# Kernel optimization log

Measured on AMD Instinct MI355X. Metric: run time of the kernel, lower is better.

## Reference

```python
import jax, jax.numpy as jnp
import numpy as np

NQ = 12          # num_qubits
NL = 5           # num_layers
NA = 4           # num_actions
DIM = 2 ** NQ    # state-vector dimension

# PennyLane convention: wire 0 is the most-significant bit of the state index.
_idx = np.arange(DIM)
_bits = (_idx[:, None] >> (NQ - 1 - np.arange(NQ))) & 1           # [DIM, NQ]
_cz = np.ones(DIM)
for _i in range(NQ):                                              # ring of CZs (all diagonal -> fuse)
    _cz *= np.where((_bits[:, _i] & _bits[:, (_i + 1) % NQ]) == 1, -1.0, 1.0)
CZ_RING = jnp.asarray(_cz, dtype=jnp.complex64)                   # [DIM]
ZTAB = jnp.asarray(1 - 2 * _bits[:, :NA], dtype=jnp.float32)      # [DIM, NA] PauliZ eigenvalues


def _bc(v):
    # broadcast an angle-derived scalar or [B] vector against [B, lead, trail]
    v = jnp.asarray(v)
    return v.reshape(v.shape + (1, 1))


def _apply_1q(state, wire, m00, m01, m10, m11):
    b = state.shape[0]
    lead, trail = 2 ** wire, 2 ** (NQ - 1 - wire)
    s = state.reshape(b, lead, 2, trail)
    s0, s1 = s[:, :, 0, :], s[:, :, 1, :]
    return jnp.stack([m00 * s0 + m01 * s1, m10 * s0 + m11 * s1], axis=2).reshape(b, DIM)


def _rx(state, wire, theta):
    c = _bc(jnp.cos(0.5 * theta)).astype(jnp.complex64)
    s = _bc(jnp.sin(0.5 * theta)).astype(jnp.complex64)
    return _apply_1q(state, wire, c, -1j * s, -1j * s, c)


def _ry(state, wire, theta):
    c = _bc(jnp.cos(0.5 * theta)).astype(jnp.complex64)
    s = _bc(jnp.sin(0.5 * theta)).astype(jnp.complex64)
    return _apply_1q(state, wire, c, -s, s, c)


def _rz(state, wire, theta):
    # diagonal gate: no mixing across the wire axis
    b = state.shape[0]
    lead, trail = 2 ** wire, 2 ** (NQ - 1 - wire)
    e = _bc(jnp.exp(-0.5j * theta))  # e^{-i t/2}; conj(e) = e^{+i t/2} for real t
    s = state.reshape(b, lead, 2, trail)
    return jnp.stack([e * s[:, :, 0, :], jnp.conj(e) * s[:, :, 1, :]], axis=2).reshape(b, DIM)


def setup_inputs() -> dict:
    key = jax.random.key(0)
    k1, k2 = jax.random.split(key)
    x = jax.random.normal(k1, (4096, 4 * NQ), dtype=jnp.float32)
    input_scaling = jnp.ones((NL, 3, NQ), dtype=jnp.float32)
    weights = jax.random.uniform(k2, (NL, 3, 2 * NQ), dtype=jnp.float32,
                                 minval=-np.pi, maxval=np.pi)
    output_scaling = jnp.ones((NA,), dtype=jnp.float32)
    return {"x": x, "input_scaling": input_scaling, "weights": weights,
            "output_scaling": output_scaling}


def reference(x, input_scaling, weights, output_scaling):
    b = x.shape[0]
    feats = (x[:, NQ:2 * NQ], x[:, 2 * NQ:3 * NQ], x[:, 3 * NQ:4 * NQ])
    state = jnp.zeros((b, DIM), dtype=jnp.complex64).at[:, 0].set(1.0)
    for layer in range(NL):
        for blk in range(3):
            f = feats[blk]
            for i in range(NQ):
                state = _rx(state, i, input_scaling[layer, blk, i] * f[:, i])
            for i in range(NQ):
                state = _ry(state, i, weights[layer, blk, i])
            for i in range(NQ):
                state = _rz(state, i, weights[layer, blk, i + NQ])
            state = state * CZ_RING[None, :]
    probs = state.real ** 2 + state.imag ** 2          # [B, DIM]
    expvals = probs @ ZTAB                             # [B, NA] <Z_i>
    return expvals * output_scaling                    # logits
```

## Files before the change

### kernel.cpp

```cpp
#include <hip/hip_runtime.h>
#include <stdint.h>

#define NQ 12
#define NL 5
#define NIT 15
#define AMPS 16
#define CPB (NIT * NQ)


typedef float f2 __attribute__((ext_vector_type(2)));

static __device__ __forceinline__ float f_u(unsigned u) { return __uint_as_float(u); }
static __device__ __forceinline__ unsigned u_f(float f) { return __float_as_uint(f); }

#define PK_MUL_RR(acc, C, S) \
    asm("v_pk_mul_f32 %0, %1, %2 op_sel_hi:[0,1]" : "=v"(acc) : "v"(C), "v"(S))
#define PK_FMA_I(acc, C, S) \
    asm("v_pk_fma_f32 %0, %1, %2, %0 op_sel:[1,1,0] op_sel_hi:[1,0,1] neg_lo:[1,0,0]" \
        : "+v"(acc) : "v"(C), "v"(S))
#define PK_FMA_R(acc, C, S) \
    asm("v_pk_fma_f32 %0, %1, %2, %0 op_sel_hi:[0,1,1]" : "+v"(acc) : "v"(C), "v"(S))
#define PK_FMA_IC(acc, C, S) \
    asm("v_pk_fma_f32 %0, %1, %2, %0 op_sel:[1,1,0] op_sel_hi:[1,0,1] neg_hi:[1,0,0]" \
        : "+v"(acc) : "v"(C), "v"(S))
#define PK_FMA_RN(acc, C, S) \
    asm("v_pk_fma_f32 %0, %1, %2, %0 op_sel_hi:[0,1,1] neg_lo:[1,0,0] neg_hi:[1,0,0]" \
        : "+v"(acc) : "v"(C), "v"(S))

#define CPLX_AB(DST, CA, S, CB, O)                                    \
    { f2 t_;                                                          \
      PK_MUL_RR(t_, CA, S); PK_FMA_I(t_, CA, S);                      \
      PK_FMA_R (t_, CB, O); PK_FMA_I(t_, CB, O);                      \
      DST = t_; }

template <int CTRL>
static __device__ __forceinline__ float dpp_xor(float v) {
    int u = (int)__float_as_uint(v);
    return __uint_as_float((unsigned)__builtin_amdgcn_update_dpp(u, u, CTRL, 0xF, 0xF, false));
}
static __device__ __forceinline__ float swz_xor4(float v) {
    return f_u((unsigned)__builtin_amdgcn_ds_swizzle((int)u_f(v), 0x101F));
}

#define AB_GATE_PK(OPX)                                                 \
    _Pragma("unroll")                                                   \
    for (int r = 0; r < AMPS; ++r) {                                    \
        f2 o; o.x = OPX(s[r].x); o.y = OPX(s[r].y);                     \
        CPLX_AB(s[r], CA, s[r], CB, o)                                  \
    }

template <int ST>
static __device__ __forceinline__ void reg_gate_pk(f2 (&s)[AMPS], f2 CAg, f2 CBg) {
#pragma unroll
    for (int r0 = 0; r0 < AMPS; ++r0) {
        if (r0 & ST) continue;
        const int r1 = r0 | ST;
        const f2 s0 = s[r0], s1 = s[r1];
        f2 t0, t1;
        PK_MUL_RR(t0, CAg, s0); PK_FMA_I (t0, CAg, s0);
        PK_FMA_R (t0, CBg, s1); PK_FMA_I (t0, CBg, s1);
        PK_MUL_RR(t1, CAg, s1); PK_FMA_IC(t1, CAg, s1);
        PK_FMA_RN(t1, CBg, s0); PK_FMA_I (t1, CBg, s0);
        s[r0] = t0; s[r1] = t1;
    }
}

static __device__ __forceinline__ float4 build_coef(float alpha, float beta, float gamma) {
    float sa, ca, sb, cb, sg, cg;
    sincosf(0.5f * alpha, &sa, &ca);
    sincosf(0.5f * beta,  &sb, &cb);
    sincosf(0.5f * gamma, &sg, &cg);
    float cbca = cb * ca, sbsa = sb * sa, sbca = sb * ca, cbsa = cb * sa;
    float ar =  cg * cbca + sg * sbsa;
    float ai =  cg * sbsa - sg * cbca;
    float br = -(cg * sbca + sg * cbsa);
    float bi =  sg * sbca - cg * cbsa;
    return make_float4(ar, ai, br, bi);
}

__global__ __launch_bounds__(256) void coef_kernel(
    const float* __restrict__ x, const float* __restrict__ iscale,
    const float* __restrict__ w, float4* __restrict__ ctab, int total)
{
    int gid = blockIdx.x * 256 + threadIdx.x;
    if (gid >= total) return;
    int b  = gid / CPB;
    int t  = gid - b * CPB;
    int it = t / NQ;
    int q  = t - it * NQ;
    int blk = it - 3 * (it / 3);
    float f     = x[(size_t)b * (4 * NQ) + NQ + blk * NQ + q];
    float alpha = iscale[it * NQ + q] * f;
    ctab[gid] = build_coef(alpha, w[it * 2 * NQ + q], w[it * 2 * NQ + NQ + q]);
}

template <bool TAB>
__global__ __launch_bounds__(256) void qsim_kernel(
    const float* __restrict__ x,
    const float* __restrict__ iscale,
    const float* __restrict__ w,
    const float* __restrict__ oscale,
    const float4* __restrict__ ctab,
    float* __restrict__ out)
{
    const int tid  = threadIdx.x;
    const int lane = tid & 63;
    const int wv   = tid >> 6;
    const int b    = blockIdx.x;

    extern __shared__ float4 smem[];
    float4* buf  = smem;
    float4* clds = smem + 1536;

#define TBUF(SLOT, Q) buf[((((SLOT) << 1) | (Q)) << 6) | lane]

    if constexpr (!TAB) {
        if (tid < CPB) {
            const int it  = tid / NQ;
            const int q   = tid - it * NQ;
            const int blk = it - 3 * (it / 3);
            float f     = x[(size_t)b * (4 * NQ) + NQ + blk * NQ + q];
            float alpha = iscale[it * NQ + q] * f;
            clds[tid] = build_coef(alpha, w[it * 2 * NQ + q], w[it * 2 * NQ + NQ + q]);
        }
        __syncthreads();
    }

    f2 s[AMPS];
#pragma unroll
    for (int r = 0; r < AMPS; ++r) { s[r].x = 0.f; s[r].y = 0.f; }
    if (tid == 0) s[0].x = 1.f;

    unsigned czmA = 0, czmB = 0;
#pragma unroll
    for (int r = 0; r < AMPS; ++r) {
        unsigned ia = ((unsigned)wv << 10) | ((unsigned)lane << 4) | (unsigned)r;
        unsigned ib = (((unsigned)(r >> 3) & 1u) << 11) | (((unsigned)(r >> 2) & 1u) << 10)
                    | ((unsigned)lane << 4)
                    | (((unsigned)(wv >> 1) & 1u) << 3) | (((unsigned)wv & 1u) << 2)
                    | ((unsigned)r & 3u);
        unsigned pa = ((unsigned)__popc((ia & (ia >> 1)) & 0x7FFu) + ((ia & (ia >> 11)) & 1u)) & 1u;
        unsigned pb = ((unsigned)__popc((ib & (ib >> 1)) & 0x7FFu) + ((ib & (ib >> 11)) & 1u)) & 1u;
        czmA |= pa << r;
        czmB |= pb << r;
    }

    const bool hb2 = (lane >> 5) & 1;
    const bool hb3 = (lane >> 4) & 1;
    const unsigned sb4 = (unsigned)((lane >> 3) & 1) << 31;
    const unsigned sb5 = (unsigned)((lane >> 2) & 1) << 31;
    const unsigned sb6 = (unsigned)((lane >> 1) & 1) << 31;
    const unsigned sb7 = (unsigned)(lane & 1) << 31;

    const float4* gtab = TAB ? (ctab + (size_t)b * CPB) : nullptr;

#pragma unroll 1
    for (int it = 0; it < NIT; ++it) {
        float4 c[NQ];
        if constexpr (TAB) {
#pragma unroll
            for (int q = 0; q < NQ; ++q) c[q] = gtab[it * NQ + q];
        } else {
#pragma unroll
            for (int q = 0; q < NQ; ++q) c[q] = clds[it * NQ + q];
        }
        const bool ev = (it & 1) == 0;

        {
            const float4 c0 = ev ? c[8] : c[0];
            const float4 c1 = ev ? c[9] : c[1];
            { const f2 CA = { c0.x, c0.y }, CB = { c0.z, c0.w }; reg_gate_pk<8>(s, CA, CB); }
            { const f2 CA = { c1.x, c1.y }, CB = { c1.z, c1.w }; reg_gate_pk<4>(s, CA, CB); }
            { const f2 CA = { c[10].x, c[10].y }, CB = { c[10].z, c[10].w }; reg_gate_pk<2>(s, CA, CB); }
            { const f2 CA = { c[11].x, c[11].y }, CB = { c[11].z, c[11].w }; reg_gate_pk<1>(s, CA, CB); }
        }

        {
            const f2 CP = { hb2 ? -c[2].z : c[2].x, hb2 ?  c[2].w : c[2].y };
            const f2 CQ = { hb2 ?  c[2].x : c[2].z, hb2 ? -c[2].y : c[2].w };
#pragma unroll
            for (int r = 0; r < AMPS; ++r) {
                auto dx = __builtin_amdgcn_permlane32_swap(u_f(s[r].x), u_f(s[r].x), false, false);
                auto dy = __builtin_amdgcn_permlane32_swap(u_f(s[r].y), u_f(s[r].y), false, false);
                f2 na = { f_u(dx[0]), f_u(dy[0]) };
                f2 nb = { f_u(dx[1]), f_u(dy[1]) };
                CPLX_AB(s[r], CP, na, CQ, nb)
            }
        }
        {
            const f2 CP = { hb3 ? -c[3].z : c[3].x, hb3 ?  c[3].w : c[3].y };
            const f2 CQ = { hb3 ?  c[3].x : c[3].z, hb3 ? -c[3].y : c[3].w };
#pragma unroll
            for (int r = 0; r < AMPS; ++r) {
                auto dx = __builtin_amdgcn_permlane16_swap(u_f(s[r].x), u_f(s[r].x), false, false);
                auto dy = __builtin_amdgcn_permlane16_swap(u_f(s[r].y), u_f(s[r].y), false, false);
                f2 na = { f_u(dx[0]), f_u(dy[0]) };
                f2 nb = { f_u(dx[1]), f_u(dy[1]) };
                CPLX_AB(s[r], CP, na, CQ, nb)
            }
        }
        {
            const f2 CA = { c[4].x, f_u(u_f(c[4].y) ^ sb4) };
            const f2 CB = { f_u(u_f(c[4].z) ^ sb4), c[4].w };
            AB_GATE_PK(dpp_xor<0x128>)
        }
        {
            const f2 CA = { c[5].x, f_u(u_f(c[5].y) ^ sb5) };
            const f2 CB = { f_u(u_f(c[5].z) ^ sb5), c[5].w };
#pragma unroll
            for (int h = 0; h < 2; ++h) {
                float ox[8], oy[8];
#pragma unroll
                for (int r = 0; r < 8; ++r) {
                    ox[r] = swz_xor4(s[h*8 + r].x);
                    oy[r] = swz_xor4(s[h*8 + r].y);
                }
#pragma unroll
                for (int r = 0; r < 8; ++r) {
                    f2 o = { ox[r], oy[r] };
                    CPLX_AB(s[h*8 + r], CA, s[h*8 + r], CB, o)
                }
            }
        }
        {
            const f2 CA = { c[6].x, f_u(u_f(c[6].y) ^ sb6) };
            const f2 CB = { f_u(u_f(c[6].z) ^ sb6), c[6].w };
            AB_GATE_PK(dpp_xor<0x4E>)
        }
        {
            const f2 CA = { c[7].x, f_u(u_f(c[7].y) ^ sb7) };
            const f2 CB = { f_u(u_f(c[7].z) ^ sb7), c[7].w };
            AB_GATE_PK(dpp_xor<0xB1>)
        }

        __syncthreads();
#pragma unroll
        for (int g = 0; g < 4; ++g) {
            if (g == wv) continue;
            const int slot = g * 3 + (wv < g ? wv : wv - 1);
            TBUF(slot, 0) = make_float4(s[4*g+0].x, s[4*g+0].y, s[4*g+1].x, s[4*g+1].y);
            TBUF(slot, 1) = make_float4(s[4*g+2].x, s[4*g+2].y, s[4*g+3].x, s[4*g+3].y);
        }
        __syncthreads();
#pragma unroll
        for (int h = 0; h < 4; ++h) {
            if (h == wv) continue;
            const int slot = wv * 3 + (h < wv ? h : h - 1);
            const float4 pa = TBUF(slot, 0);
            const float4 pb = TBUF(slot, 1);
            s[4*h+0] = f2{ pa.x, pa.y }; s[4*h+1] = f2{ pa.z, pa.w };
            s[4*h+2] = f2{ pb.x, pb.y }; s[4*h+3] = f2{ pb.z, pb.w };
        }

        {
            const float4 c0 = ev ? c[0] : c[8];
            const float4 c1 = ev ? c[1] : c[9];
            { const f2 CA = { c0.x, c0.y }, CB = { c0.z, c0.w }; reg_gate_pk<8>(s, CA, CB); }
            { const f2 CA = { c1.x, c1.y }, CB = { c1.z, c1.w }; reg_gate_pk<4>(s, CA, CB); }
        }

        const unsigned mcz = ev ? czmB : czmA;
#pragma unroll
        for (int r = 0; r < AMPS; ++r) {
            const unsigned sgn = ((mcz >> r) & 1u) << 31;
            s[r].x = f_u(u_f(s[r].x) ^ sgn);
            s[r].y = f_u(u_f(s[r].y) ^ sgn);
        }
    }

    float pg[4];
#pragma unroll
    for (int g = 0; g < 4; ++g) {
        float p = 0.f;
#pragma unroll
        for (int j = 0; j < 4; ++j)
            p = fmaf(s[4*g+j].x, s[4*g+j].x, fmaf(s[4*g+j].y, s[4*g+j].y, p));
        pg[g] = p;
    }
    const float ptot = (pg[0] + pg[1]) + (pg[2] + pg[3]);
    float v0 = (pg[0] + pg[1]) - (pg[2] + pg[3]);
    float v1 = (pg[0] + pg[2]) - (pg[1] + pg[3]);
    float v2 = hb2 ? -ptot : ptot;
    float v3 = hb3 ? -ptot : ptot;
#pragma unroll
    for (int m = 1; m <= 32; m <<= 1) {
        v0 += __shfl_xor(v0, m);
        v1 += __shfl_xor(v1, m);
        v2 += __shfl_xor(v2, m);
        v3 += __shfl_xor(v3, m);
    }

    __syncthreads();
    if (lane == 0) buf[wv] = make_float4(v0, v1, v2, v3);
    __syncthreads();
    if (tid == 0) {
        float4 a0 = buf[0], a1 = buf[1], a2 = buf[2], a3 = buf[3];
        float4 o;
        o.x = (a0.x + a1.x + a2.x + a3.x) * oscale[0];
        o.y = (a0.y + a1.y + a2.y + a3.y) * oscale[1];
        o.z = (a0.z + a1.z + a2.z + a3.z) * oscale[2];
        o.w = (a0.w + a1.w + a2.w + a3.w) * oscale[3];
        *reinterpret_cast<float4*>(out + (size_t)b * 4) = o;
    }
#undef TBUF
}

extern "C" void kernel_launch(void* const* d_in, const int* in_sizes, int n_in,
                              void* d_out, int out_size, void* d_ws, size_t ws_size,
                              hipStream_t stream) {
    const float* x      = (const float*)d_in[0];
    const float* iscale = (const float*)d_in[1];
    const float* w      = (const float*)d_in[2];
    const float* oscale = (const float*)d_in[3];
    float* out          = (float*)d_out;

    const int batch = in_sizes[0] / (4 * NQ);
    const size_t need = (size_t)batch * CPB * sizeof(float4);

    if (ws_size >= need) {
        const int total = batch * CPB;
        coef_kernel<<<(total + 255) / 256, 256, 0, stream>>>(x, iscale, w, (float4*)d_ws, total);
        qsim_kernel<true><<<batch, 256, 12 * 2 * 64 * sizeof(float4), stream>>>(
            x, iscale, w, oscale, (const float4*)d_ws, out);
    } else {
        qsim_kernel<false><<<batch, 256, (12 * 2 * 64 + CPB) * sizeof(float4), stream>>>(
            x, iscale, w, oscale, nullptr, out);
    }
}
```

Baseline: 568.8 us.

## Use 128-thread blocks with 32 amplitudes per thread and analytic first layer

Result: faster. 543.8 us (-4.4%).

```diff
diff --git a/kernel.cpp b/kernel.cpp
--- a/kernel.cpp
+++ b/kernel.cpp
@@ -2,9 +2,8 @@
 #include <stdint.h>
 
 #define NQ 12
-#define NL 5
 #define NIT 15
-#define AMPS 16
+#define AMPS 32
 #define CPB (NIT * NQ)
 
 
@@ -27,6 +26,9 @@
     asm("v_pk_fma_f32 %0, %1, %2, %0 op_sel_hi:[0,1,1] neg_lo:[1,0,0] neg_hi:[1,0,0]" \
         : "+v"(acc) : "v"(C), "v"(S))
 
+#define CMUL(DST, CA, CB) \
+    { PK_MUL_RR(DST, CA, CB); PK_FMA_I(DST, CA, CB); }
+
 #define CPLX_AB(DST, CA, S, CB, O)                                    \
     { f2 t_;                                                          \
       PK_MUL_RR(t_, CA, S); PK_FMA_I(t_, CA, S);                      \
@@ -78,29 +80,15 @@
     return make_float4(ar, ai, br, bi);
 }
 
-__global__ __launch_bounds__(256) void coef_kernel(
-    const float* __restrict__ x, const float* __restrict__ iscale,
-    const float* __restrict__ w, float4* __restrict__ ctab, int total)
-{
-    int gid = blockIdx.x * 256 + threadIdx.x;
-    if (gid >= total) return;
-    int b  = gid / CPB;
-    int t  = gid - b * CPB;
-    int it = t / NQ;
-    int q  = t - it * NQ;
-    int blk = it - 3 * (it / 3);
-    float f     = x[(size_t)b * (4 * NQ) + NQ + blk * NQ + q];
-    float alpha = iscale[it * NQ + q] * f;
-    ctab[gid] = build_coef(alpha, w[it * 2 * NQ + q], w[it * 2 * NQ + NQ + q]);
-}
-
-template <bool TAB>
-__global__ __launch_bounds__(256) void qsim_kernel(
+static __device__ __forceinline__ f2 usel(float4 c, int bit) {
+    return bit ? f2{ -c.z, c.w } : f2{ c.x, c.y };
+}
+
+__global__ __launch_bounds__(128) void qsim_kernel(
     const float* __restrict__ x,
     const float* __restrict__ iscale,
     const float* __restrict__ w,
     const float* __restrict__ oscale,
-    const float4* __restrict__ ctab,
     float* __restrict__ out)
 {
     const int tid  = threadIdx.x;
@@ -108,76 +96,98 @@
     const int wv   = tid >> 6;
     const int b    = blockIdx.x;
 
-    extern __shared__ float4 smem[];
-    float4* buf  = smem;
-    float4* clds = smem + 1536;
-
-#define TBUF(SLOT, Q) buf[((((SLOT) << 1) | (Q)) << 6) | lane]
-
-    if constexpr (!TAB) {
-        if (tid < CPB) {
-            const int it  = tid / NQ;
-            const int q   = tid - it * NQ;
-            const int blk = it - 3 * (it / 3);
-            float f     = x[(size_t)b * (4 * NQ) + NQ + blk * NQ + q];
-            float alpha = iscale[it * NQ + q] * f;
-            clds[tid] = build_coef(alpha, w[it * 2 * NQ + q], w[it * 2 * NQ + NQ + q]);
-        }
-        __syncthreads();
-    }
-
-    f2 s[AMPS];
-#pragma unroll
-    for (int r = 0; r < AMPS; ++r) { s[r].x = 0.f; s[r].y = 0.f; }
-    if (tid == 0) s[0].x = 1.f;
+    __shared__ float4 buf[8 * 128];
+    __shared__ float4 clds[CPB];
+
+    for (int t = tid; t < CPB; t += 128) {
+        const int it  = t / NQ;
+        const int q   = t - it * NQ;
+        const int blk = it - 3 * (it / 3);
+        float f     = x[(size_t)b * (4 * NQ) + NQ + blk * NQ + q];
+        float alpha = iscale[it * NQ + q] * f;
+        clds[t] = build_coef(alpha, w[it * 2 * NQ + q], w[it * 2 * NQ + NQ + q]);
+    }
 
     unsigned czmA = 0, czmB = 0;
 #pragma unroll
     for (int r = 0; r < AMPS; ++r) {
-        unsigned ia = ((unsigned)wv << 10) | ((unsigned)lane << 4) | (unsigned)r;
-        unsigned ib = (((unsigned)(r >> 3) & 1u) << 11) | (((unsigned)(r >> 2) & 1u) << 10)
-                    | ((unsigned)lane << 4)
-                    | (((unsigned)(wv >> 1) & 1u) << 3) | (((unsigned)wv & 1u) << 2)
-                    | ((unsigned)r & 3u);
+        unsigned ia = ((unsigned)wv << 11) | ((unsigned)lane << 5) | (unsigned)r;
+        unsigned ib = (((unsigned)r >> 4) << 11) | ((unsigned)lane << 5)
+                    | ((unsigned)wv << 4) | ((unsigned)r & 15u);
         unsigned pa = ((unsigned)__popc((ia & (ia >> 1)) & 0x7FFu) + ((ia & (ia >> 11)) & 1u)) & 1u;
         unsigned pb = ((unsigned)__popc((ib & (ib >> 1)) & 0x7FFu) + ((ib & (ib >> 11)) & 1u)) & 1u;
         czmA |= pa << r;
         czmB |= pb << r;
     }
 
-    const bool hb2 = (lane >> 5) & 1;
-    const bool hb3 = (lane >> 4) & 1;
-    const unsigned sb4 = (unsigned)((lane >> 3) & 1) << 31;
-    const unsigned sb5 = (unsigned)((lane >> 2) & 1) << 31;
-    const unsigned sb6 = (unsigned)((lane >> 1) & 1) << 31;
-    const unsigned sb7 = (unsigned)(lane & 1) << 31;
-
-    const float4* gtab = TAB ? (ctab + (size_t)b * CPB) : nullptr;
+    const bool hbW1 = (lane >> 5) & 1;
+    const bool hbW2 = (lane >> 4) & 1;
+    const unsigned sbW3 = (unsigned)((lane >> 3) & 1) << 31;
+    const unsigned sbW4 = (unsigned)((lane >> 2) & 1) << 31;
+    const unsigned sbW5 = (unsigned)((lane >> 1) & 1) << 31;
+    const unsigned sbW6 = (unsigned)(lane & 1) << 31;
+
+    __syncthreads();
+
+    f2 s[AMPS];
+
+    {
+        float4 c0 = clds[0], c1 = clds[1], c2 = clds[2],  c3 = clds[3];
+        float4 c4 = clds[4], c5 = clds[5], c6 = clds[6],  c7 = clds[7];
+        float4 c8 = clds[8], c9 = clds[9], cA = clds[10], cB = clds[11];
+
+        f2 tc = usel(c1, (lane >> 5) & 1);
+        { f2 u = usel(c2, (lane >> 4) & 1); f2 t; CMUL(t, tc, u) tc = t; }
+        { f2 u = usel(c3, (lane >> 3) & 1); f2 t; CMUL(t, tc, u) tc = t; }
+        { f2 u = usel(c4, (lane >> 2) & 1); f2 t; CMUL(t, tc, u) tc = t; }
+        { f2 u = usel(c5, (lane >> 1) & 1); f2 t; CMUL(t, tc, u) tc = t; }
+        { f2 u = usel(c6, lane & 1);        f2 t; CMUL(t, tc, u) tc = t; }
+        { f2 u = usel(c7, wv);              f2 t; CMUL(t, tc, u) tc = t; }
+        f2 tc0, tc1;
+        { f2 u = usel(c0, 0); CMUL(tc0, tc, u) }
+        { f2 u = usel(c0, 1); CMUL(tc1, tc, u) }
+
+        f2 pA[4], pB[4], plow[16];
+#pragma unroll
+        for (int j = 0; j < 4; ++j) {
+            f2 u8 = usel(c8, j >> 1), u9 = usel(c9, j & 1);
+            CMUL(pA[j], u8, u9)
+            f2 uA = usel(cA, j >> 1), uB = usel(cB, j & 1);
+            CMUL(pB[j], uA, uB)
+        }
+#pragma unroll
+        for (int m = 0; m < 16; ++m) CMUL(plow[m], pA[m >> 2], pB[m & 3])
+#pragma unroll
+        for (int r = 0; r < AMPS; ++r) CMUL(s[r], (r < 16 ? tc0 : tc1), plow[r & 15])
+
+#pragma unroll
+        for (int r = 0; r < AMPS; ++r) {
+            const unsigned sgn = ((czmB >> r) & 1u) << 31;
+            s[r].x = f_u(u_f(s[r].x) ^ sgn);
+            s[r].y = f_u(u_f(s[r].y) ^ sgn);
+        }
+    }
 
 #pragma unroll 1
-    for (int it = 0; it < NIT; ++it) {
-        float4 c[NQ];
-        if constexpr (TAB) {
-#pragma unroll
-            for (int q = 0; q < NQ; ++q) c[q] = gtab[it * NQ + q];
-        } else {
-#pragma unroll
-            for (int q = 0; q < NQ; ++q) c[q] = clds[it * NQ + q];
-        }
+    for (int it = 1; it < NIT; ++it) {
+        const float4* cit = clds + it * NQ;
         const bool ev = (it & 1) == 0;
 
-        {
-            const float4 c0 = ev ? c[8] : c[0];
-            const float4 c1 = ev ? c[9] : c[1];
-            { const f2 CA = { c0.x, c0.y }, CB = { c0.z, c0.w }; reg_gate_pk<8>(s, CA, CB); }
-            { const f2 CA = { c1.x, c1.y }, CB = { c1.z, c1.w }; reg_gate_pk<4>(s, CA, CB); }
-            { const f2 CA = { c[10].x, c[10].y }, CB = { c[10].z, c[10].w }; reg_gate_pk<2>(s, CA, CB); }
-            { const f2 CA = { c[11].x, c[11].y }, CB = { c[11].z, c[11].w }; reg_gate_pk<1>(s, CA, CB); }
-        }
-
-        {
-            const f2 CP = { hb2 ? -c[2].z : c[2].x, hb2 ?  c[2].w : c[2].y };
-            const f2 CQ = { hb2 ?  c[2].x : c[2].z, hb2 ? -c[2].y : c[2].w };
+        { float4 cf = cit[ev ? 7 : 0];
+          const f2 CA = { cf.x, cf.y }, CB = { cf.z, cf.w }; reg_gate_pk<16>(s, CA, CB); }
+        { float4 cc = cit[8];
+          const f2 CA = { cc.x, cc.y }, CB = { cc.z, cc.w }; reg_gate_pk<8>(s, CA, CB); }
+        { float4 cc = cit[9];
+          const f2 CA = { cc.x, cc.y }, CB = { cc.z, cc.w }; reg_gate_pk<4>(s, CA, CB); }
+        { float4 cc = cit[10];
+          const f2 CA = { cc.x, cc.y }, CB = { cc.z, cc.w }; reg_gate_pk<2>(s, CA, CB); }
+        { float4 cc = cit[11];
+          const f2 CA = { cc.x, cc.y }, CB = { cc.z, cc.w }; reg_gate_pk<1>(s, CA, CB); }
+
+        {
+            float4 cc = cit[1];
+            const f2 CP = { hbW1 ? -cc.z : cc.x, hbW1 ?  cc.w : cc.y };
+            const f2 CQ = { hbW1 ?  cc.x : cc.z, hbW1 ? -cc.y : cc.w };
 #pragma unroll
             for (int r = 0; r < AMPS; ++r) {
                 auto dx = __builtin_amdgcn_permlane32_swap(u_f(s[r].x), u_f(s[r].x), false, false);
@@ -188,8 +198,9 @@
             }
         }
         {
-            const f2 CP = { hb3 ? -c[3].z : c[3].x, hb3 ?  c[3].w : c[3].y };
-            const f2 CQ = { hb3 ?  c[3].x : c[3].z, hb3 ? -c[3].y : c[3].w };
+            float4 cc = cit[2];
+            const f2 CP = { hbW2 ? -cc.z : cc.x, hbW2 ?  cc.w : cc.y };
+            const f2 CQ = { hbW2 ?  cc.x : cc.z, hbW2 ? -cc.y : cc.w };
 #pragma unroll
             for (int r = 0; r < AMPS; ++r) {
                 auto dx = __builtin_amdgcn_permlane16_swap(u_f(s[r].x), u_f(s[r].x), false, false);
@@ -200,15 +211,17 @@
             }
         }
         {
-            const f2 CA = { c[4].x, f_u(u_f(c[4].y) ^ sb4) };
-            const f2 CB = { f_u(u_f(c[4].z) ^ sb4), c[4].w };
+            float4 cc = cit[3];
+            const f2 CA = { cc.x, f_u(u_f(cc.y) ^ sbW3) };
+            const f2 CB = { f_u(u_f(cc.z) ^ sbW3), cc.w };
             AB_GATE_PK(dpp_xor<0x128>)
         }
         {
-            const f2 CA = { c[5].x, f_u(u_f(c[5].y) ^ sb5) };
-            const f2 CB = { f_u(u_f(c[5].z) ^ sb5), c[5].w };
-#pragma unroll
-            for (int h = 0; h < 2; ++h) {
+            float4 cc = cit[4];
+            const f2 CA = { cc.x, f_u(u_f(cc.y) ^ sbW4) };
+            const f2 CB = { f_u(u_f(cc.z) ^ sbW4), cc.w };
+#pragma unroll
+            for (int h = 0; h < 4; ++h) {
                 float ox[8], oy[8];
 #pragma unroll
                 for (int r = 0; r < 8; ++r) {
@@ -223,41 +236,50 @@
             }
         }
         {
-            const f2 CA = { c[6].x, f_u(u_f(c[6].y) ^ sb6) };
-            const f2 CB = { f_u(u_f(c[6].z) ^ sb6), c[6].w };
+            float4 cc = cit[5];
+            const f2 CA = { cc.x, f_u(u_f(cc.y) ^ sbW5) };
+            const f2 CB = { f_u(u_f(cc.z) ^ sbW5), cc.w };
             AB_GATE_PK(dpp_xor<0x4E>)
         }
         {
-            const f2 CA = { c[7].x, f_u(u_f(c[7].y) ^ sb7) };
-            const f2 CB = { f_u(u_f(c[7].z) ^ sb7), c[7].w };
+            float4 cc = cit[6];
+            const f2 CA = { cc.x, f_u(u_f(cc.y) ^ sbW6) };
+            const f2 CB = { f_u(u_f(cc.z) ^ sbW6), cc.w };
             AB_GATE_PK(dpp_xor<0xB1>)
         }
 
         __syncthreads();
-#pragma unroll
-        for (int g = 0; g < 4; ++g) {
-            if (g == wv) continue;
-            const int slot = g * 3 + (wv < g ? wv : wv - 1);
-            TBUF(slot, 0) = make_float4(s[4*g+0].x, s[4*g+0].y, s[4*g+1].x, s[4*g+1].y);
-            TBUF(slot, 1) = make_float4(s[4*g+2].x, s[4*g+2].y, s[4*g+3].x, s[4*g+3].y);
+        if (wv == 0) {
+#pragma unroll
+            for (int k = 0; k < 8; ++k)
+                buf[(k << 7) + tid] = make_float4(s[16+2*k].x, s[16+2*k].y,
+                                                  s[17+2*k].x, s[17+2*k].y);
+        } else {
+#pragma unroll
+            for (int k = 0; k < 8; ++k)
+                buf[(k << 7) + tid] = make_float4(s[2*k].x, s[2*k].y,
+                                                  s[2*k+1].x, s[2*k+1].y);
         }
         __syncthreads();
-#pragma unroll
-        for (int h = 0; h < 4; ++h) {
-            if (h == wv) continue;
-            const int slot = wv * 3 + (h < wv ? h : h - 1);
-            const float4 pa = TBUF(slot, 0);
-            const float4 pb = TBUF(slot, 1);
-            s[4*h+0] = f2{ pa.x, pa.y }; s[4*h+1] = f2{ pa.z, pa.w };
-            s[4*h+2] = f2{ pb.x, pb.y }; s[4*h+3] = f2{ pb.z, pb.w };
-        }
-
-        {
-            const float4 c0 = ev ? c[0] : c[8];
-            const float4 c1 = ev ? c[1] : c[9];
-            { const f2 CA = { c0.x, c0.y }, CB = { c0.z, c0.w }; reg_gate_pk<8>(s, CA, CB); }
-            { const f2 CA = { c1.x, c1.y }, CB = { c1.z, c1.w }; reg_gate_pk<4>(s, CA, CB); }
-        }
+        {
+            const int ptid = tid ^ 64;
+            if (wv == 0) {
+#pragma unroll
+                for (int k = 0; k < 8; ++k) {
+                    float4 v = buf[(k << 7) + ptid];
+                    s[16+2*k] = f2{ v.x, v.y }; s[17+2*k] = f2{ v.z, v.w };
+                }
+            } else {
+#pragma unroll
+                for (int k = 0; k < 8; ++k) {
+                    float4 v = buf[(k << 7) + ptid];
+                    s[2*k] = f2{ v.x, v.y }; s[2*k+1] = f2{ v.z, v.w };
+                }
+            }
+        }
+
+        { float4 cl = cit[ev ? 0 : 7];
+          const f2 CA = { cl.x, cl.y }, CB = { cl.z, cl.w }; reg_gate_pk<16>(s, CA, CB); }
 
         const unsigned mcz = ev ? czmB : czmA;
 #pragma unroll
@@ -268,20 +290,17 @@
         }
     }
 
-    float pg[4];
-#pragma unroll
-    for (int g = 0; g < 4; ++g) {
-        float p = 0.f;
-#pragma unroll
-        for (int j = 0; j < 4; ++j)
-            p = fmaf(s[4*g+j].x, s[4*g+j].x, fmaf(s[4*g+j].y, s[4*g+j].y, p));
-        pg[g] = p;
-    }
-    const float ptot = (pg[0] + pg[1]) + (pg[2] + pg[3]);
-    float v0 = (pg[0] + pg[1]) - (pg[2] + pg[3]);
-    float v1 = (pg[0] + pg[2]) - (pg[1] + pg[3]);
-    float v2 = hb2 ? -ptot : ptot;
-    float v3 = hb3 ? -ptot : ptot;
+    float plo = 0.f, phi = 0.f;
+#pragma unroll
+    for (int r = 0; r < 16; ++r) plo = fmaf(s[r].x, s[r].x, fmaf(s[r].y, s[r].y, plo));
+#pragma unroll
+    for (int r = 16; r < 32; ++r) phi = fmaf(s[r].x, s[r].x, fmaf(s[r].y, s[r].y, phi));
+
+    const float ptot = plo + phi;
+    float v0 = plo - phi;
+    float v1 = hbW1 ? -ptot : ptot;
+    float v2 = hbW2 ? -ptot : ptot;
+    float v3 = ((lane >> 3) & 1) ? -ptot : ptot;
 #pragma unroll
     for (int m = 1; m <= 32; m <<= 1) {
         v0 += __shfl_xor(v0, m);
@@ -294,15 +313,14 @@
     if (lane == 0) buf[wv] = make_float4(v0, v1, v2, v3);
     __syncthreads();
     if (tid == 0) {
-        float4 a0 = buf[0], a1 = buf[1], a2 = buf[2], a3 = buf[3];
+        float4 a0 = buf[0], a1 = buf[1];
         float4 o;
-        o.x = (a0.x + a1.x + a2.x + a3.x) * oscale[0];
-        o.y = (a0.y + a1.y + a2.y + a3.y) * oscale[1];
-        o.z = (a0.z + a1.z + a2.z + a3.z) * oscale[2];
-        o.w = (a0.w + a1.w + a2.w + a3.w) * oscale[3];
+        o.x = (a0.x + a1.x) * oscale[0];
+        o.y = (a0.y + a1.y) * oscale[1];
+        o.z = (a0.z + a1.z) * oscale[2];
+        o.w = (a0.w + a1.w) * oscale[3];
         *reinterpret_cast<float4*>(out + (size_t)b * 4) = o;
     }
-#undef TBUF
 }
 
 extern "C" void kernel_launch(void* const* d_in, const int* in_sizes, int n_in,
@@ -315,15 +333,5 @@
     float* out          = (float*)d_out;
 
     const int batch = in_sizes[0] / (4 * NQ);
-    const size_t need = (size_t)batch * CPB * sizeof(float4);
-
-    if (ws_size >= need) {
-        const int total = batch * CPB;
-        coef_kernel<<<(total + 255) / 256, 256, 0, stream>>>(x, iscale, w, (float4*)d_ws, total);
-        qsim_kernel<true><<<batch, 256, 12 * 2 * 64 * sizeof(float4), stream>>>(
-            x, iscale, w, oscale, (const float4*)d_ws, out);
-    } else {
-        qsim_kernel<false><<<batch, 256, (12 * 2 * 64 + CPB) * sizeof(float4), stream>>>(
-            x, iscale, w, oscale, nullptr, out);
-    }
-}
+    qsim_kernel<<<batch, 128, 0, stream>>>(x, iscale, w, oscale, out);
+}
```
